# Optimization experiments

Measured on AMD Instinct MI355X. Metric: run time of the kernel, lower is better.

Reference implementation:

```python
import jax, jax.numpy as jnp
from jax import lax
import numpy as np

# ---- constants matching init_kwargs ----
STEPSZ = 0.1
ALPHA = 0.01
BETA = 0.01
FLTRSTDEV = 2.0
NSTEPS = 20
DMAX = 15.0
EXTGRADFAC = 10.0
THRESH = 0.5
B, H, W = 4, 384, 384
NNODES = 64
ANGLE_STEP = 10  # degrees, as in the source


def make_gauss_edge_fltr(std):
    """Derivative-of-Gaussian edge filters, one per spatial dim -> [2,1,k,k]."""
    r = int(4 * std)
    x = jnp.arange(-r, r + 1, dtype=jnp.float32)
    g = jnp.exp(-0.5 * (x / std) ** 2)
    g = g / g.sum()
    dg = -(x / std ** 2) * jnp.exp(-0.5 * (x / std) ** 2)
    f0 = dg[:, None] * g[None, :]   # d/d(row)
    f1 = g[:, None] * dg[None, :]   # d/d(col)
    return jnp.stack([f0, f1])[:, None]  # [2,1,k,k]


def make_Ainv(n, alpha, beta, stepsz):
    """Implicit-Euler snake internal-energy matrix inverse (I + t*A)^-1 (static)."""
    D1 = np.zeros((n - 1, n), dtype=np.float64)
    for i in range(n - 1):
        D1[i, i], D1[i, i + 1] = -1.0, 1.0
    D2 = np.zeros((n - 2, n), dtype=np.float64)
    for i in range(n - 2):
        D2[i, i], D2[i, i + 1], D2[i, i + 2] = 1.0, -2.0, 1.0
    A = alpha * (D1.T @ D1) + beta * (D2.T @ D2)
    return jnp.asarray(np.linalg.inv(np.eye(n) + stepsz * A), dtype=np.float32)


def bilinear(img, pts):
    """img [C,H,W], pts [N,2] (row,col) -> [N,C] bilinear samples."""
    C, Hh, Ww = img.shape
    x = jnp.clip(pts[:, 0], 0.0, Hh - 1.0)
    y = jnp.clip(pts[:, 1], 0.0, Ww - 1.0)
    x0 = jnp.clip(jnp.floor(x).astype(jnp.int32), 0, Hh - 2)
    y0 = jnp.clip(jnp.floor(y).astype(jnp.int32), 0, Ww - 2)
    fx = (x - x0)[None, :]
    fy = (y - y0)[None, :]
    v00 = img[:, x0, y0]
    v01 = img[:, x0, y0 + 1]
    v10 = img[:, x0 + 1, y0]
    v11 = img[:, x0 + 1, y0 + 1]
    top = v00 * (1 - fy) + v01 * fy
    bot = v10 * (1 - fy) + v11 * fy
    return (top * (1 - fx) + bot * fx).T


def radial_widths(prob, nodes):
    """Vectorized version of the nested r/angle scan: for each node, smallest
    radius r whose ring has an in-bounds pixel with prob < 0.5 -> width r-1;
    if the ring first goes out of bounds with no hit -> width 0."""
    angles = jnp.radians(jnp.arange(0, 360, ANGLE_STEP, dtype=jnp.float32))  # [A]
    rs = jnp.arange(1, H, dtype=jnp.float32)                                 # [R]
    sx = jnp.round(nodes[:, 0])[:, None, None]
    sy = jnp.round(nodes[:, 1])[:, None, None]
    ox = rs[:, None] * jnp.cos(angles)[None, :]  # [R,A]
    oy = rs[:, None] * jnp.sin(angles)[None, :]
    xi = jnp.floor(sx + ox[None]).astype(jnp.int32)  # [N,R,A]
    yi = jnp.floor(sy + oy[None]).astype(jnp.int32)
    inb = (xi >= 0) & (xi < H) & (yi >= 0) & (yi < W)
    p = prob[jnp.clip(xi, 0, H - 1), jnp.clip(yi, 0, W - 1)]
    hit = jnp.any(inb & (p < THRESH), axis=-1)   # [N,R]
    oob = jnp.any(~inb, axis=-1)                 # [N,R]
    stop = hit | oob
    idx = jnp.argmax(stop, axis=-1)              # first stopping radius index
    trig = jnp.any(stop, axis=-1)
    hit_at = jnp.take_along_axis(hit, idx[:, None], axis=-1)[:, 0]
    return jnp.where(trig & hit_at, rs[idx] - 1.0, 0.0)  # [N]


def render_maps(nodes, widths, dmax):
    """Per-pixel min distance to polyline edges (clipped at dmax) and a
    ribbon mask where distance <= linearly-interpolated width."""
    p0, p1 = nodes[:-1], nodes[1:]          # [E,2]
    w0, w1 = widths[:-1], widths[1:]        # [E]
    gx, gy = jnp.meshgrid(jnp.arange(H, dtype=jnp.float32),
                          jnp.arange(W, dtype=jnp.float32), indexing='ij')
    pts = jnp.stack([gx.ravel(), gy.ravel()], axis=-1)  # [P,2]
    v = p1 - p0
    vv = jnp.sum(v * v, axis=-1) + 1e-8
    d = pts[:, None, :] - p0[None, :, :]                # [P,E,2]
    t = jnp.clip(jnp.sum(d * v[None], axis=-1) / vv[None], 0.0, 1.0)  # [P,E]
    proj = p0[None] + t[..., None] * v[None]
    dist = jnp.sqrt(jnp.sum((pts[:, None, :] - proj) ** 2, axis=-1) + 1e-12)
    wt = w0[None] + t * (w1 - w0)[None]
    dmap = jnp.minimum(jnp.min(dist, axis=-1), dmax).reshape(H, W)
    pmap = (jnp.min(dist - wt, axis=-1) <= 0.0).astype(jnp.float32).reshape(H, W)
    return dmap, pmap


def setup_inputs() -> dict:
    key = jax.random.key(0)
    k1, k2 = jax.random.split(key)
    pred_dmap = jax.random.normal(k1, (B, 1, H, W), dtype=jnp.float32)
    # smooth polyline snakes: diagonal-ish curve + jitter, kept in-bounds
    t = jnp.linspace(0.1, 0.9, NNODES)
    base_x = t * (H - 1)
    base_y = (0.5 + 0.2 * jnp.sin(2 * jnp.pi * t)) * (W - 1)
    jitter = (jax.random.uniform(k2, (B, NNODES, 2)) - 0.5) * 8.0
    snake_init = jnp.stack([jnp.broadcast_to(base_x, (B, NNODES)),
                            jnp.broadcast_to(base_y, (B, NNODES))], axis=-1) + jitter
    snake_init = jnp.clip(snake_init, 2.0, H - 3.0).astype(jnp.float32)
    return {"pred_dmap": pred_dmap, "snake_init": snake_init}


def reference(pred_dmap, snake_init):
    fltr = make_gauss_edge_fltr(FLTRSTDEV)
    # gradient image of the predicted distance map, scaled by extgradfac
    gimg = lax.conv_general_dilated(
        pred_dmap, fltr, (1, 1), 'SAME',
        dimension_numbers=('NCHW', 'OIHW', 'NCHW')) * EXTGRADFAC  # [B,2,H,W]
    Ainv = make_Ainv(NNODES, ALPHA, BETA, STEPSZ)

    def per_sample(g, pred_i, nodes0):
        def step(pos, _):
            f = bilinear(g, pos)                     # external force [N,2]
            return Ainv @ (pos + STEPSZ * f), None
        pos, _ = lax.scan(step, nodes0, None, length=NSTEPS)
        prob = jax.nn.sigmoid(-pred_i[0])            # [H,W]
        w = radial_widths(prob, pos)
        return render_maps(pos, w, DMAX)

    dmaps, pmaps = jax.vmap(per_sample)(gimg, pred_dmap, snake_init)
    snake_dm = dmaps[:, None]   # [B,1,H,W]
    ribbon_pm = pmaps[:, None]
    loss = jnp.mean((pred_dmap - snake_dm) ** 2)
    loss = loss + jnp.mean((jax.nn.sigmoid(pred_dmap) - ribbon_pm) ** 2)
    return loss
```

## Files before the change

kernel.cpp:

```cpp
#include <hip/hip_runtime.h>

#define Hh 384
#define Ww 384
#define Bb 4
#define NN 64
#define HW (Hh*Ww)
#define NSEG (NN-1)
#define TPB 24
#define NTILES (TPB*TPB)

struct AinvT { float a[NN][NN]; };
constexpr AinvT make_ainv() {
    AinvT R{};
    float d[NN] = {}, u1[NN] = {}, u2[NN] = {}, b1[NN] = {}, L1[NN] = {}, L2[NN] = {};
    for (int k = 0; k < NN-1; ++k) { d[k] += 0.01f; d[k+1] += 0.01f; u1[k] -= 0.01f; }
    for (int k = 0; k < NN-2; ++k) {
        d[k] += 0.01f; d[k+1] += 0.04f; d[k+2] += 0.01f;
        u1[k] -= 0.02f; u1[k+1] -= 0.02f; u2[k] += 0.01f;
    }
    for (int k = 0; k < NN; ++k) {
        d[k]  = 1.0f + 0.1f*d[k];
        u1[k] = 0.1f*u1[k];
        u2[k] = 0.1f*u2[k];
        b1[k] = u1[k];
    }
    for (int k = 0; k < NN; ++k) {
        float di = d[k];
        if (k+1 < NN) { float l = b1[k]/di; L1[k] = l; d[k+1] -= l*u1[k]; if (k+2 < NN) u1[k+1] -= l*u2[k]; }
        if (k+2 < NN) { float l = u2[k]/di; L2[k] = l; b1[k+1] -= l*u1[k]; d[k+2] -= l*u2[k]; }
    }
    for (int t = 0; t < NN; ++t) {
        float y[NN] = {}, x[NN] = {};
        for (int k = 0; k < NN; ++k) {
            float v = (k == t) ? 1.0f : 0.0f;
            if (k >= 1) v -= L1[k-1]*y[k-1];
            if (k >= 2) v -= L2[k-2]*y[k-2];
            y[k] = v;
        }
        for (int kk = 0; kk < NN; ++kk) {
            int k = NN-1-kk;
            float v = y[k];
            if (k+1 < NN) v -= u1[k]*x[k+1];
            if (k+2 < NN) v -= u2[k]*x[k+2];
            x[k] = v/d[k];
        }
        for (int k = 0; k < NN; ++k) R.a[k][t] = x[k];
    }
    return R;
}
__device__ constexpr AinvT g_Ainv = make_ainv();

#define TILE 32
#define HALO 8
__global__ __launch_bounds__(256) void k_conv(const float* __restrict__ img,
        float2* __restrict__ gimg) {
    __shared__ float sIn[TILE+2*HALO][TILE+2*HALO];
    __shared__ float sColG[TILE+2*HALO][TILE];
    __shared__ float sColD[TILE+2*HALO][TILE];
    __shared__ float gtap[17], dtap[17];
    const int b  = blockIdx.z;
    const int x0 = blockIdx.x * TILE;
    const int y0 = blockIdx.y * TILE;
    const int tid = threadIdx.x;
    if (tid == 0) {
        float s = 0.f;
        for (int i = 0; i < 17; ++i) {
            float xv = (float)(i - 8);
            float e  = expf(-0.5f * (xv*0.5f)*(xv*0.5f));
            gtap[i] = e; s += e;
            dtap[i] = -(xv*0.25f) * e;
        }
        for (int i = 0; i < 17; ++i) gtap[i] /= s;
    }
    const float* im = img + b*HW;
    for (int idx = tid; idx < 48*48; idx += blockDim.x) {
        int r = idx / 48, c = idx % 48;
        int gx = x0 + r - HALO, gy = y0 + c - HALO;
        float v = 0.f;
        if (gx >= 0 && gx < Hh && gy >= 0 && gy < Ww) v = im[gx*Ww + gy];
        sIn[r][c] = v;
    }
    __syncthreads();
    for (int idx = tid; idx < 48*TILE; idx += blockDim.x) {
        int r = idx / TILE, c = idx % TILE;
        float ag = 0.f, ad = 0.f;
#pragma unroll
        for (int k = 0; k < 17; ++k) {
            float v = sIn[r][c+k];
            ag += gtap[k]*v;
            ad += dtap[k]*v;
        }
        sColG[r][c] = ag; sColD[r][c] = ad;
    }
    __syncthreads();
    float2* gg = gimg + (size_t)b*HW;
    for (int idx = tid; idx < TILE*TILE; idx += blockDim.x) {
        int xo = idx / TILE, c = idx % TILE;
        float a0 = 0.f, a1 = 0.f;
#pragma unroll
        for (int k = 0; k < 17; ++k) {
            a0 += dtap[k]*sColG[xo+k][c];
            a1 += gtap[k]*sColD[xo+k][c];
        }
        int gx = x0+xo, gy = y0+c;
        gg[gx*Ww+gy] = make_float2(10.f*a0, 10.f*a1);
    }
}

__global__ __launch_bounds__(256) void k_snake(const float2* __restrict__ gimg,
                        const float* __restrict__ pred, const float* __restrict__ init,
                        float4* __restrict__ pA, float4* __restrict__ pB) {
    __shared__ float2 stxy[NN];
    __shared__ float swf[NN];
    const int b = blockIdx.x;
    const int tid = threadIdx.x;
    const int i = tid >> 2;
    const int q = tid & 3;

    float ar[16];
#pragma unroll
    for (int k = 0; k < 16; ++k) ar[k] = g_Ainv.a[i][q*16 + k];

    float px = init[(b*NN + i)*2 + 0];
    float py = init[(b*NN + i)*2 + 1];
    const float2* g = gimg + (size_t)b*HW;

    for (int s = 0; s < 20; ++s) {
        float x = fminf(fmaxf(px, 0.f), (float)(Hh-1));
        float y = fminf(fmaxf(py, 0.f), (float)(Ww-1));
        int x0i = (int)floorf(x); x0i = min(max(x0i, 0), Hh-2);
        int y0i = (int)floorf(y); y0i = min(max(y0i, 0), Ww-2);
        float fx = x - (float)x0i, fy = y - (float)y0i;
        int base = x0i*Ww + y0i;
        if (q == 0) {
            float2 v00 = g[base],    v01 = g[base+1];
            float2 v10 = g[base+Ww], v11 = g[base+Ww+1];
            float t0x = v00.x*(1.f-fy) + v01.x*fy;
            float t0y = v00.y*(1.f-fy) + v01.y*fy;
            float b0x = v10.x*(1.f-fy) + v11.x*fy;
            float b0y = v10.y*(1.f-fy) + v11.y*fy;
            float f0 = t0x*(1.f-fx) + b0x*fx;
            float f1 = t0y*(1.f-fx) + b0y*fx;
            stxy[i] = make_float2(px + 0.1f*f0, py + 0.1f*f1);
        }
        __syncthreads();
        float ax = 0.f, ay = 0.f;
#pragma unroll
        for (int k = 0; k < 16; ++k) {
            float2 tv = stxy[q*16 + k];
            ax = fmaf(ar[k], tv.x, ax);
            ay = fmaf(ar[k], tv.y, ay);
        }
        ax += __shfl_xor(ax, 1); ay += __shfl_xor(ay, 1);
        ax += __shfl_xor(ax, 2); ay += __shfl_xor(ay, 2);
        px = ax; py = ay;
        __syncthreads();
    }
    if (q == 0) stxy[i] = make_float2(px, py);
    __syncthreads();

    const float* p = pred + (size_t)b*HW;
    const int wid  = tid >> 6;
    const int lane = tid & 63;
    const bool active = lane < 36;
    const float theta = (float)(10*lane) * 0.017453292519943295f;
    const float cth = cosf(theta), sth = sinf(theta);

    float v1[16];
    unsigned inbm = 0u;
#pragma unroll
    for (int nc = 0; nc < 16; ++nc) {
        const int node = wid*16 + nc;
        const float sx = rintf(stxy[node].x);
        const float sy = rintf(stxy[node].y);
        int xi = (int)floorf(sx + cth);
        int yi = (int)floorf(sy + sth);
        bool inb = (xi >= 0) & (xi < Hh) & (yi >= 0) & (yi < Ww);
        inbm |= (inb ? 1u : 0u) << nc;
        int cx = min(max(xi, 0), Hh-1);
        int cy = min(max(yi, 0), Ww-1);
        v1[nc] = p[cx*Ww + cy];
    }
#pragma unroll
    for (int nc = 0; nc < 16; ++nc) {
        const int node = wid*16 + nc;
        bool inb = (inbm >> nc) & 1u;
        bool hit = active && inb && (v1[nc] > 0.f);
        bool oob = active && !inb;
        unsigned long long mh = __ballot(hit);
        unsigned long long mo = __ballot(oob);
        float w = 0.f;
        if (!(mh | mo)) {
            const float sx = rintf(stxy[node].x);
            const float sy = rintf(stxy[node].y);
            for (int r = 2; r < Hh; ++r) {
                float rf = (float)r;
                bool hit2 = false, oob2 = false;
                if (active) {
                    int xi = (int)floorf(sx + rf*cth);
                    int yi = (int)floorf(sy + rf*sth);
                    bool inb2 = (xi >= 0) & (xi < Hh) & (yi >= 0) & (yi < Ww);
                    if (!inb2) oob2 = true;
                    else if (p[xi*Ww + yi] > 0.f) hit2 = true;
                }
                unsigned long long mh2 = __ballot(hit2);
                unsigned long long mo2 = __ballot(oob2);
                if (mh2 | mo2) { w = mh2 ? (rf - 1.f) : 0.f; break; }
            }
        }
        if (lane == 0) swf[node] = w;
    }
    __syncthreads();

    if (tid < NSEG) {
        float2 P0 = stxy[tid], P1 = stxy[tid+1];
        float vx = P1.x - P0.x, vy = P1.y - P0.y;
        float vv = vx*vx + vy*vy + 1e-8f;
        float w0 = swf[tid], w1 = swf[tid+1];
        pA[b*NSEG + tid] = make_float4(P0.x, P0.y, vx, vy);
        pB[b*NSEG + tid] = make_float4(1.0f/vv, w0, w1 - w0, 0.f);
    }
}

__global__ __launch_bounds__(256) void k_render(const float* __restrict__ pred,
                        const float4* __restrict__ pAg, const float4* __restrict__ pBg,
                        float* __restrict__ partial) {
    __shared__ float4 sSa[NSEG], sSb[NSEG];
    __shared__ int slist[NSEG];
    __shared__ int scount;
    __shared__ float red[256];
    const int b   = blockIdx.z;
    const int tid = threadIdx.x;
    const int row0 = blockIdx.x * 16, col0 = blockIdx.y * 16;
    if (tid == 0) scount = 0;
    if (tid < NSEG) {
        sSa[tid] = pAg[b*NSEG + tid];
        sSb[tid] = pBg[b*NSEG + tid];
    }
    __syncthreads();
    if (tid < NSEG) {
        const float4 A = sSa[tid];
        const float4 Bv = sSb[tid];
        float cx = (float)row0 + 7.5f, cy = (float)col0 + 7.5f;
        float dx = cx - A.x, dy = cy - A.y;
        float t = fmaf(dy, A.w, dx*A.z) * Bv.x;
        t = fminf(fmaxf(t, 0.f), 1.f);
        float ex = fmaf(-t, A.z, dx);
        float ey = fmaf(-t, A.w, dy);
        float dc = sqrtf(ex*ex + ey*ey);
        float wmax = fmaxf(Bv.y, Bv.y + Bv.z);
        float lim = fmaxf(15.0f, wmax) + 10.6066f + 0.05f;
        if (dc <= lim) {
            int idx = atomicAdd(&scount, 1);
            slist[idx] = tid;
        }
    }
    __syncthreads();
    const int cnt = scount;
    const int r = tid >> 4, c = tid & 15;
    const float fx = (float)(row0 + r), fy = (float)(col0 + c);
    float m1 = 1e30f, m2 = 1e30f;
    for (int k = 0; k < cnt; ++k) {
        const int s2 = slist[k];
        const float4 A = sSa[s2];
        const float4 Bv = sSb[s2];
        float dx = fx - A.x, dy = fy - A.y;
        float t = fmaf(dy, A.w, dx*A.z) * Bv.x;
        t = fminf(fmaxf(t, 0.f), 1.f);
        float ex = fmaf(-t, A.z, dx);
        float ey = fmaf(-t, A.w, dy);
        float d2 = fmaf(ex, ex, fmaf(ey, ey, 1e-12f));
        float wt = fmaf(t, Bv.z, Bv.y);
        m1 = fminf(m1, d2);
        m2 = fminf(m2, fmaf(-wt, wt, d2));
    }
    float dmap = fminf(sqrtf(m1), 15.f);
    float pm = (m2 <= 0.f) ? 1.f : 0.f;
    float pv = pred[(size_t)b*HW + (row0 + r)*Ww + (col0 + c)];
    float sg = 1.f/(1.f + expf(-pv));
    float t1 = pv - dmap, t2 = sg - pm;
    red[tid] = t1*t1 + t2*t2;
    __syncthreads();
    for (int off = 128; off > 0; off >>= 1) {
        if (tid < off) red[tid] += red[tid+off];
        __syncthreads();
    }
    if (tid == 0)
        partial[b*NTILES + blockIdx.y*TPB + blockIdx.x] = red[0];
}

__global__ void k_final(const float* __restrict__ partial, float* __restrict__ out, int n) {
    __shared__ double red[256];
    const int tid = threadIdx.x;
    double a = 0.0;
    for (int i = tid; i < n; i += 256) a += (double)partial[i];
    red[tid] = a; __syncthreads();
    for (int off = 128; off > 0; off >>= 1) {
        if (tid < off) red[tid] += red[tid+off];
        __syncthreads();
    }
    if (tid == 0) out[0] = (float)(red[0] / (double)((size_t)Bb*HW));
}

extern "C" void kernel_launch(void* const* d_in, const int* in_sizes, int n_in,
                              void* d_out, int out_size, void* d_ws, size_t ws_size,
                              hipStream_t stream) {
    const float* pred = (const float*)d_in[0];
    const float* init = (const float*)d_in[1];
    float* out = (float*)d_out;
    char* ws = (char*)d_ws;
    float4* pA     = (float4*)(ws);
    float4* pB     = (float4*)(ws + 4096);
    float* partial = (float*)(ws + 19456);
    float2* gimg   = (float2*)(ws + 28672);

    k_conv  <<<dim3(12,12,4),     dim3(256), 0, stream>>>(pred, gimg);
    k_snake <<<dim3(4),           dim3(256), 0, stream>>>(gimg, pred, init, pA, pB);
    k_render<<<dim3(TPB,TPB,Bb),  dim3(256), 0, stream>>>(pred, pA, pB, partial);
    k_final <<<dim3(1),           dim3(256), 0, stream>>>(partial, out, Bb*NTILES);
}
```

Measured before the change: 39.90 us.

## Compute gradient force on demand at snake nodes instead of full-image convolution

Removes the full-image separable derivative-of-Gaussian convolution kernel. The snake kernel now computes the bilinearly interpolated gradient directly at each node by folding the bilinear weights into 18x18 filter taps and summing over the pred rows, with the rows split across four threads per node. This drops a whole kernel launch and the full gradient-image write and read. In exchange, the serial 20-step snake loop, which runs on only 4 blocks, does more arithmetic and more scattered global loads per step.

New measurement: 87.00 us. +118.0%, slower.

```diff
diff --git a/kernel.cpp b/kernel.cpp
--- a/kernel.cpp
+++ b/kernel.cpp
@@ -50,72 +50,34 @@
 }
 __device__ constexpr AinvT g_Ainv = make_ainv();
 
-#define TILE 32
-#define HALO 8
-__global__ __launch_bounds__(256) void k_conv(const float* __restrict__ img,
-        float2* __restrict__ gimg) {
-    __shared__ float sIn[TILE+2*HALO][TILE+2*HALO];
-    __shared__ float sColG[TILE+2*HALO][TILE];
-    __shared__ float sColD[TILE+2*HALO][TILE];
-    __shared__ float gtap[17], dtap[17];
-    const int b  = blockIdx.z;
-    const int x0 = blockIdx.x * TILE;
-    const int y0 = blockIdx.y * TILE;
-    const int tid = threadIdx.x;
-    if (tid == 0) {
-        float s = 0.f;
-        for (int i = 0; i < 17; ++i) {
-            float xv = (float)(i - 8);
-            float e  = expf(-0.5f * (xv*0.5f)*(xv*0.5f));
-            gtap[i] = e; s += e;
-            dtap[i] = -(xv*0.25f) * e;
-        }
-        for (int i = 0; i < 17; ++i) gtap[i] /= s;
-    }
-    const float* im = img + b*HW;
-    for (int idx = tid; idx < 48*48; idx += blockDim.x) {
-        int r = idx / 48, c = idx % 48;
-        int gx = x0 + r - HALO, gy = y0 + c - HALO;
-        float v = 0.f;
-        if (gx >= 0 && gx < Hh && gy >= 0 && gy < Ww) v = im[gx*Ww + gy];
-        sIn[r][c] = v;
-    }
-    __syncthreads();
-    for (int idx = tid; idx < 48*TILE; idx += blockDim.x) {
-        int r = idx / TILE, c = idx % TILE;
-        float ag = 0.f, ad = 0.f;
-#pragma unroll
-        for (int k = 0; k < 17; ++k) {
-            float v = sIn[r][c+k];
-            ag += gtap[k]*v;
-            ad += dtap[k]*v;
-        }
-        sColG[r][c] = ag; sColD[r][c] = ad;
-    }
-    __syncthreads();
-    float2* gg = gimg + (size_t)b*HW;
-    for (int idx = tid; idx < TILE*TILE; idx += blockDim.x) {
-        int xo = idx / TILE, c = idx % TILE;
-        float a0 = 0.f, a1 = 0.f;
-#pragma unroll
-        for (int k = 0; k < 17; ++k) {
-            a0 += dtap[k]*sColG[xo+k][c];
-            a1 += gtap[k]*sColD[xo+k][c];
-        }
-        int gx = x0+xo, gy = y0+c;
-        gg[gx*Ww+gy] = make_float2(10.f*a0, 10.f*a1);
-    }
-}
-
-__global__ __launch_bounds__(256) void k_snake(const float2* __restrict__ gimg,
-                        const float* __restrict__ pred, const float* __restrict__ init,
+__global__ __launch_bounds__(256) void k_snake(const float* __restrict__ pred,
+                        const float* __restrict__ init,
                         float4* __restrict__ pA, float4* __restrict__ pB) {
     __shared__ float2 stxy[NN];
     __shared__ float swf[NN];
+    __shared__ float sg[17], sdg[17];
+    __shared__ float ssum;
     const int b = blockIdx.x;
     const int tid = threadIdx.x;
     const int i = tid >> 2;
     const int q = tid & 3;
+    const float* p = pred + (size_t)b*HW;
+
+    if (tid < 17) {
+        float xv = (float)(tid - 8);
+        float e  = expf(-0.5f * (xv*0.5f)*(xv*0.5f));
+        sg[tid]  = e;
+        sdg[tid] = -(xv*0.25f) * e;
+    }
+    __syncthreads();
+    if (tid == 0) {
+        float s = 0.f;
+        for (int k = 0; k < 17; ++k) s += sg[k];
+        ssum = s;
+    }
+    __syncthreads();
+    if (tid < 17) sg[tid] /= ssum;
+    __syncthreads();
 
     float ar[16];
 #pragma unroll
@@ -123,7 +85,6 @@
 
     float px = init[(b*NN + i)*2 + 0];
     float py = init[(b*NN + i)*2 + 1];
-    const float2* g = gimg + (size_t)b*HW;
 
     for (int s = 0; s < 20; ++s) {
         float x = fminf(fmaxf(px, 0.f), (float)(Hh-1));
@@ -131,18 +92,61 @@
         int x0i = (int)floorf(x); x0i = min(max(x0i, 0), Hh-2);
         int y0i = (int)floorf(y); y0i = min(max(y0i, 0), Ww-2);
         float fx = x - (float)x0i, fy = y - (float)y0i;
-        int base = x0i*Ww + y0i;
-        if (q == 0) {
-            float2 v00 = g[base],    v01 = g[base+1];
-            float2 v10 = g[base+Ww], v11 = g[base+Ww+1];
-            float t0x = v00.x*(1.f-fy) + v01.x*fy;
-            float t0y = v00.y*(1.f-fy) + v01.y*fy;
-            float b0x = v10.x*(1.f-fy) + v11.x*fy;
-            float b0y = v10.y*(1.f-fy) + v11.y*fy;
-            float f0 = t0x*(1.f-fx) + b0x*fx;
-            float f1 = t0y*(1.f-fx) + b0y*fx;
-            stxy[i] = make_float2(px + 0.1f*f0, py + 0.1f*f1);
-        }
+
+        float Wyg[18], Wyd[18];
+#pragma unroll
+        for (int t = 0; t < 18; ++t) {
+            float a0 = (t < 17) ? sg[t]  : 0.f;
+            float a1 = (t >= 1) ? sg[t-1]  : 0.f;
+            float d0 = (t < 17) ? sdg[t] : 0.f;
+            float d1 = (t >= 1) ? sdg[t-1] : 0.f;
+            Wyg[t] = (1.f-fy)*a0 + fy*a1;
+            Wyd[t] = (1.f-fy)*d0 + fy*d1;
+        }
+        const int ybase = y0i - 8;
+        const bool fastcol = (ybase >= 0) && (y0i + 9 < Ww);
+
+        float f0 = 0.f, f1 = 0.f;
+#pragma unroll
+        for (int k = 0; k < 5; ++k) {
+            int srow = q + 4*k;
+            if (srow < 18) {
+                int xr = x0i + srow - 8;
+                float rs_g = 0.f, rs_d = 0.f;
+                if (xr >= 0 && xr < Hh) {
+                    const float* rowp = p + xr*Ww + ybase;
+                    if (fastcol) {
+#pragma unroll
+                        for (int t = 0; t < 18; ++t) {
+                            float v = rowp[t];
+                            rs_g = fmaf(Wyg[t], v, rs_g);
+                            rs_d = fmaf(Wyd[t], v, rs_d);
+                        }
+                    } else {
+#pragma unroll
+                        for (int t = 0; t < 18; ++t) {
+                            int yc = ybase + t;
+                            float v = (yc >= 0 && yc < Ww) ? p[xr*Ww + yc] : 0.f;
+                            rs_g = fmaf(Wyg[t], v, rs_g);
+                            rs_d = fmaf(Wyd[t], v, rs_d);
+                        }
+                    }
+                }
+                float xg0 = (srow < 17) ? sg[srow]  : 0.f;
+                float xg1 = (srow >= 1) ? sg[srow-1]  : 0.f;
+                float xd0 = (srow < 17) ? sdg[srow] : 0.f;
+                float xd1 = (srow >= 1) ? sdg[srow-1] : 0.f;
+                float wxg = (1.f-fx)*xg0 + fx*xg1;
+                float wxd = (1.f-fx)*xd0 + fx*xd1;
+                f0 = fmaf(wxd, rs_g, f0);
+                f1 = fmaf(wxg, rs_d, f1);
+            }
+        }
+        f0 += __shfl_xor(f0, 1); f1 += __shfl_xor(f1, 1);
+        f0 += __shfl_xor(f0, 2); f1 += __shfl_xor(f1, 2);
+        float tx = px + 0.1f*(f0*10.f);
+        float ty = py + 0.1f*(f1*10.f);
+        if (q == 0) stxy[i] = make_float2(tx, ty);
         __syncthreads();
         float ax = 0.f, ay = 0.f;
 #pragma unroll
@@ -159,7 +163,6 @@
     if (q == 0) stxy[i] = make_float2(px, py);
     __syncthreads();
 
-    const float* p = pred + (size_t)b*HW;
     const int wid  = tid >> 6;
     const int lane = tid & 63;
     const bool active = lane < 36;
@@ -312,10 +315,8 @@
     float4* pA     = (float4*)(ws);
     float4* pB     = (float4*)(ws + 4096);
     float* partial = (float*)(ws + 19456);
-    float2* gimg   = (float2*)(ws + 28672);
-
-    k_conv  <<<dim3(12,12,4),     dim3(256), 0, stream>>>(pred, gimg);
-    k_snake <<<dim3(4),           dim3(256), 0, stream>>>(gimg, pred, init, pA, pB);
+
+    k_snake <<<dim3(4),           dim3(256), 0, stream>>>(pred, init, pA, pB);
     k_render<<<dim3(TPB,TPB,Bb),  dim3(256), 0, stream>>>(pred, pA, pB, partial);
     k_final <<<dim3(1),           dim3(256), 0, stream>>>(partial, out, Bb*NTILES);
 }
```
